# Kernel tuning notes

Measured on AMD Instinct MI355X. Metric: run time of the kernel, lower is better.

Reference implementation:

```python
import jax, jax.numpy as jnp
import numpy as np
import math

D_MODEL = 128

def setup_inputs() -> dict:
    key = jax.random.key(0)
    k0, k1, k2, k3, k4 = jax.random.split(key, 5)
    B, T, H, W, C = 1, 256, 32, 32, D_MODEL
    x = jax.random.normal(k0, (B, T, H, W, C), jnp.float32)
    dt = jax.random.uniform(k1, (B, T), jnp.float32)
    # freq_init = exp(linspace(log 1, log 100, C)); log_freq = linspace(0, log 100, C)
    log_freq = jnp.linspace(0.0, math.log(100.0), C).astype(jnp.float32)
    W_in = jax.random.normal(k2, (2 * C, C), jnp.float32) / np.float32(np.sqrt(C))
    W_out = jax.random.normal(k3, (C, 2 * C), jnp.float32) / np.float32(np.sqrt(2 * C))
    b_out = 0.01 * jax.random.normal(k4, (C,), jnp.float32)
    return {"x": x, "dt": dt, "log_freq": log_freq, "W_in": W_in, "W_out": W_out, "b_out": b_out}


def reference(x, dt, log_freq, W_in, W_out, b_out):
    # Faithful jax port of HamiltonianPropagator.forward_parallel with
    # conserve_energy=True (decay=0, |A|=1) and initial_state=None.
    B, T, H, W_, C = x.shape
    HW = H * W_
    # (B,T,H,W,C) -> (B*HW, T, C): each spatial site is an independent sequence
    x_flat = x.reshape(B, T, HW, C).transpose(0, 2, 1, 3).reshape(B * HW, T, C)
    dt_flat = jnp.broadcast_to(dt[:, None, :, None], (B, HW, T, 1)).reshape(B * HW, T, 1)
    # Evolution operator A = exp(i * freq * dt) (unit magnitude, energy conserved)
    freq = jnp.exp(log_freq)              # (C,)
    phase = freq * dt_flat                # (N,T,C)
    A = jax.lax.complex(jnp.cos(phase), jnp.sin(phase))
    # Input projection -> complex forcing, scaled by dt
    x_proj = jnp.einsum('ntc,dc->ntd', x_flat, W_in)   # (N,T,2C)
    x_r, x_i = jnp.split(x_proj, 2, axis=-1)
    X_val = jax.lax.complex(x_r, x_i) * dt_flat        # (N,T,C) complex
    # Diagonal complex linear recurrence h_t = A_t h_{t-1} + X_t via associative scan
    def comb(e1, e2):
        a1, b1 = e1
        a2, b2 = e2
        return a2 * a1, a2 * b1 + b2
    _, h_states = jax.lax.associative_scan(comb, (A, X_val), axis=1)  # (N,T,C)
    h_final = h_states[:, -1, :].reshape(B, H, W_, C)
    h_cat = jnp.concatenate([h_states.real, h_states.imag], axis=-1)  # (N,T,2C)
    out = jnp.einsum('ntd,cd->ntc', h_cat, W_out) + b_out             # (N,T,C)
    out = out.reshape(B, HW, T, C).transpose(0, 2, 1, 3).reshape(B, T, H, W_, C)
    return out, h_final
```

## Files before the change

kernel.cpp:

```cpp
#include <hip/hip_runtime.h>
#include <hip/hip_bf16.h>


typedef __attribute__((ext_vector_type(8))) short bf16x8;
typedef __attribute__((ext_vector_type(4))) float f32x4;
typedef __attribute__((ext_vector_type(2))) float f32x2;

#define T_DIM 256
#define N_SEQ 1024
#define C_DIM 128
#define SLAB  16
#define NSLAB 16
#define XPST  260
#define OUT0  (256u * 1024u * 128u)
#define HF_N  (N_SEQ * C_DIM)

__device__ __forceinline__ short f2bf(float f) {
    union { float f; unsigned u; } v; v.f = f;
    unsigned r = (v.u + 0x7FFFu + ((v.u >> 16) & 1u)) >> 16;
    return (short)(unsigned short)r;
}

__device__ __forceinline__ bf16x8 pack8(f32x4 a, f32x4 b) {
    bf16x8 f;
    f[0] = f2bf(a[0]); f[1] = f2bf(a[1]); f[2] = f2bf(a[2]); f[3] = f2bf(a[3]);
    f[4] = f2bf(b[0]); f[5] = f2bf(b[1]); f[6] = f2bf(b[2]); f[7] = f2bf(b[3]);
    return f;
}

__global__ void k_scan(const float* __restrict__ dt, float* __restrict__ Ddt) {
    __shared__ double s[T_DIM];
    int t = threadIdx.x;
    float d = dt[t];
    s[t] = (double)d;
    __syncthreads();
    for (int off = 1; off < T_DIM; off <<= 1) {
        double add = (t >= off) ? s[t - off] : 0.0;
        __syncthreads();
        s[t] += add;
        __syncthreads();
    }
    Ddt[2 * t]     = (float)s[t];
    Ddt[2 * t + 1] = d;
}

__global__ __launch_bounds__(256, 2) void k_main(
    const float* __restrict__ x, const float* __restrict__ W_in,
    const float* __restrict__ W_out, const float* __restrict__ b_out,
    const float* __restrict__ log_freq, const float* __restrict__ Ddt,
    float* __restrict__ out, int write_imag)
{
    __shared__ __align__(16) short lds_x[2][SLAB * C_DIM];
    __shared__ __align__(16) float lds_xp[SLAB * XPST];
    __shared__ __align__(16) short lds_h[SLAB * 2 * C_DIM];
    __shared__ __align__(8)  f32x2 lds_ddt[T_DIM];

    const int n    = blockIdx.x;
    const int tid  = threadIdx.x;
    const int lane = tid & 63;
    const int wv   = tid >> 6;
    const int lrow = lane & 15;
    const int lgrp = lane >> 4;

    lds_ddt[tid] = *(const f32x2*)(Ddt + 2 * tid);

    const float frev = (float)(exp((double)log_freq[tid & 127]) * 0.15915494309189535);

    bf16x8 B1[4][4];
#pragma unroll
    for (int s = 0; s < 4; ++s)
#pragma unroll
        for (int t = 0; t < 4; ++t) {
            int col = wv * 64 + t * 16 + lrow;
            int k0  = s * 32 + lgrp * 8;
            const float* p = W_in + (size_t)col * C_DIM + k0;
            B1[s][t] = pack8(*(const f32x4*)p, *(const f32x4*)(p + 4));
        }
    bf16x8 B2[8][2];
#pragma unroll
    for (int s = 0; s < 8; ++s)
#pragma unroll
        for (int t = 0; t < 2; ++t) {
            int col = wv * 32 + t * 16 + lrow;
            int k0  = s * 32 + lgrp * 8;
            const float* p = W_out + (size_t)col * (2 * C_DIM) + k0;
            B2[s][t] = pack8(*(const f32x4*)p, *(const f32x4*)(p + 4));
        }
    float bo0 = b_out[wv * 32 + lrow];
    float bo1 = b_out[wv * 32 + 16 + lrow];

    float Sr = 0.f, Si = 0.f;
    const int trow = tid >> 4, cg = tid & 15;
    const int sbyte = trow * 256 + ((cg * 16) ^ ((trow & 7) << 4));

    f32x4 pf0, pf1;
    {
        const float* p = x + ((size_t)trow * N_SEQ + n) * C_DIM + cg * 8;
        pf0 = *(const f32x4*)p;
        pf1 = *(const f32x4*)(p + 4);
    }
    *(bf16x8*)((char*)lds_x[0] + sbyte) = pack8(pf0, pf1);
    {
        const float* p = x + ((size_t)(SLAB + trow) * N_SEQ + n) * C_DIM + cg * 8;
        pf0 = *(const f32x4*)p;
        pf1 = *(const f32x4*)(p + 4);
    }
    __syncthreads();

    for (int slab = 0; slab < NSLAB; ++slab) {
        const int t0 = slab * SLAB;

        f32x4 acc1[4];
#pragma unroll
        for (int t = 0; t < 4; ++t) acc1[t] = (f32x4){0.f, 0.f, 0.f, 0.f};
#pragma unroll
        for (int s = 0; s < 4; ++s) {
            int ab = lrow * 256 + ((s * 64 + lgrp * 16) ^ ((lrow & 7) << 4));
            bf16x8 af = *(const bf16x8*)((const char*)lds_x[slab & 1] + ab);
#pragma unroll
            for (int t = 0; t < 4; ++t)
                acc1[t] = __builtin_amdgcn_mfma_f32_16x16x32_bf16(af, B1[s][t], acc1[t], 0, 0, 0);
        }

        if (slab < NSLAB - 1)
            *(bf16x8*)((char*)lds_x[(slab + 1) & 1] + sbyte) = pack8(pf0, pf1);
        if (slab < NSLAB - 2) {
            const float* p = x + ((size_t)(t0 + 2 * SLAB + trow) * N_SEQ + n) * C_DIM + cg * 8;
            pf0 = *(const f32x4*)p;
            pf1 = *(const f32x4*)(p + 4);
        }

#pragma unroll
        for (int t = 0; t < 4; ++t)
#pragma unroll
            for (int r = 0; r < 4; ++r)
                lds_xp[(lgrp * 4 + r) * XPST + wv * 64 + t * 16 + lrow] = acc1[t][r];
        __syncthreads();

        if (tid < C_DIM) {
            __builtin_amdgcn_s_setprio(1);
#pragma unroll
            for (int tt = 0; tt < SLAB; ++tt) {
                f32x2 dd = lds_ddt[t0 + tt];
                float rev = frev * dd[0];
                rev -= floorf(rev);
                float sp, cp;
                asm("v_sin_f32 %0, %1" : "=v"(sp) : "v"(rev));
                asm("v_cos_f32 %0, %1" : "=v"(cp) : "v"(rev));
                float q2 = cp * dd[1], q3 = sp * dd[1];
                float xr = lds_xp[tt * XPST + tid];
                float xi = lds_xp[tt * XPST + C_DIM + tid];
                Sr += q2 * xr + q3 * xi;
                Si += q2 * xi - q3 * xr;
                float hr = cp * Sr - sp * Si;
                float hi = sp * Sr + cp * Si;
                int swz = (tt & 7) << 4;
                *(short*)((char*)lds_h + tt * 512 + ((tid * 2) ^ swz))             = f2bf(hr);
                *(short*)((char*)lds_h + tt * 512 + (((C_DIM + tid) * 2) ^ swz))   = f2bf(hi);
                if (t0 + tt == T_DIM - 1) {
                    out[OUT0 + (size_t)n * C_DIM + tid] = hr;
                    if (write_imag)
                        out[OUT0 + HF_N + (size_t)n * C_DIM + tid] = hi;
                }
            }
            __builtin_amdgcn_s_setprio(0);
        }
        __syncthreads();

        f32x4 acc2[2];
        acc2[0] = (f32x4){0.f, 0.f, 0.f, 0.f};
        acc2[1] = (f32x4){0.f, 0.f, 0.f, 0.f};
#pragma unroll
        for (int s = 0; s < 8; ++s) {
            int ab = lrow * 512 + ((s * 64 + lgrp * 16) ^ ((lrow & 7) << 4));
            bf16x8 af = *(const bf16x8*)((const char*)lds_h + ab);
#pragma unroll
            for (int t = 0; t < 2; ++t)
                acc2[t] = __builtin_amdgcn_mfma_f32_16x16x32_bf16(af, B2[s][t], acc2[t], 0, 0, 0);
        }
#pragma unroll
        for (int r = 0; r < 4; ++r) {
            size_t row = (size_t)(t0 + lgrp * 4 + r);
            out[(row * N_SEQ + n) * C_DIM + wv * 32 + lrow]      = acc2[0][r] + bo0;
            out[(row * N_SEQ + n) * C_DIM + wv * 32 + 16 + lrow] = acc2[1][r] + bo1;
        }
    }
}

extern "C" void kernel_launch(void* const* d_in, const int* in_sizes, int n_in,
                              void* d_out, int out_size, void* d_ws, size_t ws_size,
                              hipStream_t stream) {
    const float* x        = (const float*)d_in[0];
    const float* dt       = (const float*)d_in[1];
    const float* log_freq = (const float*)d_in[2];
    const float* W_in     = (const float*)d_in[3];
    const float* W_out    = (const float*)d_in[4];
    const float* b_out    = (const float*)d_in[5];
    float* out = (float*)d_out;

    float* Ddt = (float*)d_ws;

    int write_imag = (out_size >= (int)(OUT0 + 2u * HF_N)) ? 1 : 0;

    k_scan<<<1, T_DIM, 0, stream>>>(dt, Ddt);
    k_main<<<N_SEQ, 256, 0, stream>>>(x, W_in, W_out, b_out, log_freq, Ddt, out, write_imag);
}
```

Measured before the change: 132.5 us.

## Precompute per-timestep phase rotation table in prologue kernel, replace syncthreads with lgkm barrier

The cos/sin rotation and dt-scaled coefficients depend only on (t, c), not on the sequence index, so a 16-block prologue kernel now computes a T×C table of float4 {cos, sin, cos·dt, sin·dt} in double-precision phase. The main kernel's serial scan reads that table from global/L2 instead of evaluating transcendentals per step, shortening the latency-bound critical path. __syncthreads is also replaced by a barrier that only waits on LDS counters, so the outstanding global prefetch loads are not drained at each barrier. The cost is a 512KB table read from L2 inside the serial loop, whose load latency could now sit on the critical path.

```diff
diff --git a/kernel.cpp b/kernel.cpp
--- a/kernel.cpp
+++ b/kernel.cpp
@@ -4,7 +4,6 @@
 
 typedef __attribute__((ext_vector_type(8))) short bf16x8;
 typedef __attribute__((ext_vector_type(4))) float f32x4;
-typedef __attribute__((ext_vector_type(2))) float f32x2;
 
 #define T_DIM 256
 #define N_SEQ 1024
@@ -28,11 +27,22 @@
     return f;
 }
 
-__global__ void k_scan(const float* __restrict__ dt, float* __restrict__ Ddt) {
+__device__ __forceinline__ void barrier_l() {
+    asm volatile("s_waitcnt lgkmcnt(0)" ::: "memory");
+    __builtin_amdgcn_s_barrier();
+    asm volatile("" ::: "memory");
+}
+
+__global__ void k_scan(const float* __restrict__ dt,
+                       const float* __restrict__ log_freq,
+                       f32x4* __restrict__ tbl) {
     __shared__ double s[T_DIM];
+    __shared__ double frevd[C_DIM];
     int t = threadIdx.x;
     float d = dt[t];
     s[t] = (double)d;
+    if (t < C_DIM)
+        frevd[t] = exp((double)log_freq[t]) * 0.15915494309189535;
     __syncthreads();
     for (int off = 1; off < T_DIM; off <<= 1) {
         double add = (t >= off) ? s[t - off] : 0.0;
@@ -40,20 +50,34 @@
         s[t] += add;
         __syncthreads();
     }
-    Ddt[2 * t]     = (float)s[t];
-    Ddt[2 * t + 1] = d;
+    int row  = blockIdx.x * 16 + (t >> 4);
+    int cgrp = t & 15;
+    double D  = s[row];
+    float dtf = dt[row];
+#pragma unroll
+    for (int j = 0; j < 8; ++j) {
+        int c = cgrp * 8 + j;
+        double rev = frevd[c] * D;
+        rev -= floor(rev);
+        float rf = (float)rev;
+        float sp, cp;
+        asm("v_sin_f32 %0, %1" : "=v"(sp) : "v"(rf));
+        asm("v_cos_f32 %0, %1" : "=v"(cp) : "v"(rf));
+        f32x4 e;
+        e[0] = cp; e[1] = sp; e[2] = cp * dtf; e[3] = sp * dtf;
+        tbl[(size_t)row * C_DIM + c] = e;
+    }
 }
 
 __global__ __launch_bounds__(256, 2) void k_main(
     const float* __restrict__ x, const float* __restrict__ W_in,
     const float* __restrict__ W_out, const float* __restrict__ b_out,
-    const float* __restrict__ log_freq, const float* __restrict__ Ddt,
+    const f32x4* __restrict__ tbl,
     float* __restrict__ out, int write_imag)
 {
     __shared__ __align__(16) short lds_x[2][SLAB * C_DIM];
     __shared__ __align__(16) float lds_xp[SLAB * XPST];
     __shared__ __align__(16) short lds_h[SLAB * 2 * C_DIM];
-    __shared__ __align__(8)  f32x2 lds_ddt[T_DIM];
 
     const int n    = blockIdx.x;
     const int tid  = threadIdx.x;
@@ -62,10 +86,6 @@
     const int lrow = lane & 15;
     const int lgrp = lane >> 4;
 
-    lds_ddt[tid] = *(const f32x2*)(Ddt + 2 * tid);
-
-    const float frev = (float)(exp((double)log_freq[tid & 127]) * 0.15915494309189535);
-
     bf16x8 B1[4][4];
 #pragma unroll
     for (int s = 0; s < 4; ++s)
@@ -105,7 +125,7 @@
         pf0 = *(const f32x4*)p;
         pf1 = *(const f32x4*)(p + 4);
     }
-    __syncthreads();
+    barrier_l();
 
     for (int slab = 0; slab < NSLAB; ++slab) {
         const int t0 = slab * SLAB;
@@ -135,25 +155,20 @@
 #pragma unroll
             for (int r = 0; r < 4; ++r)
                 lds_xp[(lgrp * 4 + r) * XPST + wv * 64 + t * 16 + lrow] = acc1[t][r];
-        __syncthreads();
+        barrier_l();
 
         if (tid < C_DIM) {
             __builtin_amdgcn_s_setprio(1);
+            const f32x4* tb = tbl + (size_t)t0 * C_DIM + tid;
 #pragma unroll
             for (int tt = 0; tt < SLAB; ++tt) {
-                f32x2 dd = lds_ddt[t0 + tt];
-                float rev = frev * dd[0];
-                rev -= floorf(rev);
-                float sp, cp;
-                asm("v_sin_f32 %0, %1" : "=v"(sp) : "v"(rev));
-                asm("v_cos_f32 %0, %1" : "=v"(cp) : "v"(rev));
-                float q2 = cp * dd[1], q3 = sp * dd[1];
+                f32x4 q = tb[(size_t)tt * C_DIM];
                 float xr = lds_xp[tt * XPST + tid];
                 float xi = lds_xp[tt * XPST + C_DIM + tid];
-                Sr += q2 * xr + q3 * xi;
-                Si += q2 * xi - q3 * xr;
-                float hr = cp * Sr - sp * Si;
-                float hi = sp * Sr + cp * Si;
+                Sr = fmaf(q[2], xr, fmaf(q[3], xi, Sr));
+                Si = fmaf(q[2], xi, fmaf(-q[3], xr, Si));
+                float hr = q[0] * Sr - q[1] * Si;
+                float hi = q[1] * Sr + q[0] * Si;
                 int swz = (tt & 7) << 4;
                 *(short*)((char*)lds_h + tt * 512 + ((tid * 2) ^ swz))             = f2bf(hr);
                 *(short*)((char*)lds_h + tt * 512 + (((C_DIM + tid) * 2) ^ swz))   = f2bf(hi);
@@ -165,7 +180,7 @@
             }
             __builtin_amdgcn_s_setprio(0);
         }
-        __syncthreads();
+        barrier_l();
 
         f32x4 acc2[2];
         acc2[0] = (f32x4){0.f, 0.f, 0.f, 0.f};
@@ -198,10 +213,10 @@
     const float* b_out    = (const float*)d_in[5];
     float* out = (float*)d_out;
 
-    float* Ddt = (float*)d_ws;
+    f32x4* tbl = (f32x4*)d_ws;
 
     int write_imag = (out_size >= (int)(OUT0 + 2u * HF_N)) ? 1 : 0;
 
-    k_scan<<<1, T_DIM, 0, stream>>>(dt, Ddt);
-    k_main<<<N_SEQ, 256, 0, stream>>>(x, W_in, W_out, b_out, log_freq, Ddt, out, write_imag);
-}
+    k_scan<<<16, T_DIM, 0, stream>>>(dt, log_freq, tbl);
+    k_main<<<N_SEQ, 256, 0, stream>>>(x, W_in, W_out, b_out, tbl, out, write_imag);
+}
```

After: 140.7 us. 1.06x slower.
